# Performance work log

Hardware: AMD Instinct MI355X
Metric: run time of the kernel (lower is better)

The kernel has to match this reference:

```python
import jax, jax.numpy as jnp
import numpy as np

B, S, D, H = 4, 2048, 1024, 16
DK = D // H


def setup_inputs() -> dict:
    key = jax.random.key(0)
    ks = jax.random.split(key, 5)
    scale = 1.0 / np.sqrt(D)
    return {
        "x": jax.random.normal(ks[0], (B, S, D), dtype=jnp.float32),
        "W_Q": jax.random.normal(ks[1], (D, D), dtype=jnp.float32) * scale,
        "W_K": jax.random.normal(ks[2], (D, D), dtype=jnp.float32) * scale,
        "W_V": jax.random.normal(ks[3], (D, D), dtype=jnp.float32) * scale,
        "W_O": jax.random.normal(ks[4], (D, D), dtype=jnp.float32) * scale,
    }


def reference(x, W_Q, W_K, W_V, W_O):
    b, s, d = x.shape
    # torch Linear convention: y = x @ W.T  (no bias in this assignment's Linear)
    q = (x @ W_Q.T).reshape(b, s, H, DK).transpose(0, 2, 1, 3)  # [b,h,s,dk]
    k = (x @ W_K.T).reshape(b, s, H, DK).transpose(0, 2, 1, 3)
    v = (x @ W_V.T).reshape(b, s, H, DK).transpose(0, 2, 1, 3)
    scores = jnp.einsum("bhqd,bhkd->bhqk", q, k) / jnp.sqrt(jnp.float32(DK))
    causal = jnp.tril(jnp.ones((s, s), dtype=bool))  # True where attention allowed
    scores = jnp.where(causal, scores, jnp.finfo(scores.dtype).min)
    attn = jax.nn.softmax(scores, axis=-1)
    out = jnp.einsum("bhqk,bhkd->bhqd", attn, v)
    out = out.transpose(0, 2, 1, 3).reshape(b, s, d)
    return out @ W_O.T
```

## Files before the change

### kernel.cpp

```cpp
#include <hip/hip_runtime.h>
#include <hip/hip_bf16.h>

#define BB 4
#define SS 2048
#define DD 1024
#define HH 16
#define DKK 64

typedef __attribute__((ext_vector_type(8))) short short8;
typedef __attribute__((ext_vector_type(4))) float f32x4;

typedef const __attribute__((address_space(1))) void gvoid;
typedef __attribute__((address_space(3))) void lvoid;

__device__ __forceinline__ unsigned short f2bf(float f) {
  unsigned int u = __builtin_bit_cast(unsigned int, f);
  u = (u + 0x7FFFu + ((u >> 16) & 1u)) >> 16;
  return (unsigned short)u;
}

__global__ __launch_bounds__(256) void convert_f32_bf16(
    const float* __restrict__ in, unsigned short* __restrict__ out, int n4) {
  int i = blockIdx.x * blockDim.x + threadIdx.x;
  if (i >= n4) return;
  float4 v = reinterpret_cast<const float4*>(in)[i];
  ushort4 o;
  o.x = f2bf(v.x); o.y = f2bf(v.y); o.z = f2bf(v.z); o.w = f2bf(v.w);
  reinterpret_cast<ushort4*>(out)[i] = o;
}

template<int MODE>
__global__ __launch_bounds__(256) void gemm_bt(
    const unsigned short* __restrict__ A,
    const unsigned short* __restrict__ Bm,
    void* __restrict__ C,
    int M, int N, int K, float scale)
{
  __shared__ unsigned short As[128 * 32];
  __shared__ unsigned short Bs[128 * 32];
  int bid = blockIdx.x;
  int ntn = N >> 7;
  int m0 = (bid / ntn) << 7;
  int n0 = (bid % ntn) << 7;
  int t = threadIdx.x;
  int lane = t & 63, w = t >> 6;
  int l16 = lane & 15, lhi = lane >> 4;
  int wm = (w >> 1) * 64, wn = (w & 1) * 64;

  f32x4 acc[4][4];
#pragma unroll
  for (int i = 0; i < 4; ++i)
#pragma unroll
    for (int j = 0; j < 4; ++j) acc[i][j] = (f32x4){0.f, 0.f, 0.f, 0.f};

  for (int kt = 0; kt < K; kt += 32) {
    __syncthreads();
#pragma unroll
    for (int is = 0; is < 2; ++is) {
      int c = is * 256 + t;
      __builtin_amdgcn_global_load_lds(
          (gvoid*)(A + (size_t)(m0 + (c >> 2)) * K + kt + ((c & 3) << 3)),
          (lvoid*)(As + (size_t)(is * 256 + w * 64) * 8), 16, 0, 0);
      __builtin_amdgcn_global_load_lds(
          (gvoid*)(Bm + (size_t)(n0 + (c >> 2)) * K + kt + ((c & 3) << 3)),
          (lvoid*)(Bs + (size_t)(is * 256 + w * 64) * 8), 16, 0, 0);
    }
    __syncthreads();
    short8 af[4], bfr[4];
#pragma unroll
    for (int mf = 0; mf < 4; ++mf)
      af[mf] = *(const short8*)(As + (wm + mf * 16 + l16) * 32 + lhi * 8);
#pragma unroll
    for (int nf = 0; nf < 4; ++nf)
      bfr[nf] = *(const short8*)(Bs + (wn + nf * 16 + l16) * 32 + lhi * 8);
#pragma unroll
    for (int mf = 0; mf < 4; ++mf)
#pragma unroll
      for (int nf = 0; nf < 4; ++nf)
        acc[mf][nf] = __builtin_amdgcn_mfma_f32_16x16x32_bf16(
            af[mf], bfr[nf], acc[mf][nf], 0, 0, 0);
  }

  if (MODE == 0) {
    unsigned short* out = (unsigned short*)C;
#pragma unroll
    for (int mf = 0; mf < 4; ++mf)
#pragma unroll
      for (int nf = 0; nf < 4; ++nf)
#pragma unroll
        for (int i = 0; i < 4; ++i) {
          int r = m0 + wm + mf * 16 + lhi * 4 + i;
          int cc = n0 + wn + nf * 16 + l16;
          int b = r >> 11, s = r & 2047;
          int h = cc >> 6, dk = cc & 63;
          out[((size_t)((b * HH + h) * SS + s) << 6) + dk] =
              f2bf(acc[mf][nf][i] * scale);
        }
  } else if (MODE == 2) {
    unsigned short* out = (unsigned short*)C;
#pragma unroll
    for (int mf = 0; mf < 4; ++mf)
#pragma unroll
      for (int nf = 0; nf < 4; ++nf)
#pragma unroll
        for (int i = 0; i < 4; ++i) {
          int r = m0 + wm + mf * 16 + lhi * 4 + i;
          int cc = n0 + wn + nf * 16 + l16;
          int b = r >> 11, s = r & 2047;
          int h = cc >> 6, dk = cc & 63;
          out[(size_t)((b * HH + h) * DKK + dk) * SS + s] =
              f2bf(acc[mf][nf][i] * scale);
        }
  } else {
    float* out = (float*)C;
#pragma unroll
    for (int mf = 0; mf < 4; ++mf)
#pragma unroll
      for (int nf = 0; nf < 4; ++nf)
#pragma unroll
        for (int i = 0; i < 4; ++i) {
          int r = m0 + wm + mf * 16 + lhi * 4 + i;
          int cc = n0 + wn + nf * 16 + l16;
          out[(size_t)r * N + cc] = acc[mf][nf][i];
        }
  }
}

__global__ __launch_bounds__(256, 2) void attn_kernel(
    const unsigned short* __restrict__ Qh,
    const unsigned short* __restrict__ Kh,
    const unsigned short* __restrict__ Vt,
    unsigned short* __restrict__ O)
{
  __shared__ unsigned short Plds[4][32 * 72];

  int bid = blockIdx.x;
  int bh = bid & 63;
  int qb = 15 - (bid >> 6);
  int q0 = qb << 7;
  int t = threadIdx.x, lane = t & 63, w = t >> 6;
  int l16 = lane & 15, lhi = lane >> 4;
  int wq0 = q0 + w * 32;

  const unsigned short* Qb = Qh + (size_t)bh * SS * DKK;
  const unsigned short* Kb = Kh + (size_t)bh * SS * DKK;
  const unsigned short* Vb = Vt + (size_t)bh * SS * DKK;

  short8 aq[2][2];
#pragma unroll
  for (int qf = 0; qf < 2; ++qf)
#pragma unroll
    for (int kc = 0; kc < 2; ++kc)
      aq[qf][kc] = *(const short8*)(Qb + (size_t)(wq0 + qf * 16 + l16) * DKK +
                                    kc * 32 + lhi * 8);

  f32x4 oacc[2][4], acc1[2];
#pragma unroll
  for (int qf = 0; qf < 2; ++qf) {
    acc1[qf] = (f32x4){0.f, 0.f, 0.f, 0.f};
#pragma unroll
    for (int d = 0; d < 4; ++d) oacc[qf][d] = (f32x4){0.f, 0.f, 0.f, 0.f};
  }

  short8 ones;
  {
    short ov = (l16 == 0) ? (short)0x3F80 : (short)0;
#pragma unroll
    for (int j = 0; j < 8; ++j) ones[j] = ov;
  }

  int nt = (wq0 >> 6) + 1;

  short8 bk[4][2], bv[4][2];
#pragma unroll
  for (int sf = 0; sf < 4; ++sf)
#pragma unroll
    for (int kc = 0; kc < 2; ++kc)
      bk[sf][kc] = *(const short8*)(Kb + (size_t)(sf * 16 + l16) * DKK +
                                    kc * 32 + lhi * 8);
#pragma unroll
  for (int d = 0; d < 4; ++d)
#pragma unroll
    for (int kc = 0; kc < 2; ++kc)
      bv[d][kc] = *(const short8*)(Vb + (size_t)(d * 16 + l16) * SS +
                                   kc * 32 + lhi * 8);

  for (int tt = 0; tt < nt; ++tt) {
    int kv0 = tt << 6;
    f32x4 sacc[2][4];
#pragma unroll
    for (int qf = 0; qf < 2; ++qf)
#pragma unroll
      for (int sf = 0; sf < 4; ++sf) {
        sacc[qf][sf] = (f32x4){0.f, 0.f, 0.f, 0.f};
        sacc[qf][sf] = __builtin_amdgcn_mfma_f32_16x16x32_bf16(
            aq[qf][0], bk[sf][0], sacc[qf][sf], 0, 0, 0);
        sacc[qf][sf] = __builtin_amdgcn_mfma_f32_16x16x32_bf16(
            aq[qf][1], bk[sf][1], sacc[qf][sf], 0, 0, 0);
      }
    if (tt + 1 < nt) {
      int nk = kv0 + 64;
#pragma unroll
      for (int sf = 0; sf < 4; ++sf)
#pragma unroll
        for (int kc = 0; kc < 2; ++kc)
          bk[sf][kc] = *(const short8*)(Kb + (size_t)(nk + sf * 16 + l16) * DKK +
                                        kc * 32 + lhi * 8);
    }
    bool lastT = (tt == nt - 1);
#pragma unroll
    for (int qf = 0; qf < 2; ++qf)
#pragma unroll
      for (int sf = 0; sf < 4; ++sf)
#pragma unroll
        for (int i = 0; i < 4; ++i) {
          float p = exp2f(sacc[qf][sf][i] - 16.0f);
          if (lastT) {
            int key = kv0 + sf * 16 + l16;
            int qr = wq0 + qf * 16 + lhi * 4 + i;
            if (key > qr) p = 0.f;
          }
          Plds[w][(qf * 16 + lhi * 4 + i) * 72 + sf * 16 + l16] = f2bf(p);
        }
    short8 ap[2][2];
#pragma unroll
    for (int qf = 0; qf < 2; ++qf)
#pragma unroll
      for (int kc = 0; kc < 2; ++kc)
        ap[qf][kc] = *(const short8*)(&Plds[w][(qf * 16 + l16) * 72 + kc * 32 + lhi * 8]);
#pragma unroll
    for (int qf = 0; qf < 2; ++qf)
#pragma unroll
      for (int kc = 0; kc < 2; ++kc)
        acc1[qf] = __builtin_amdgcn_mfma_f32_16x16x32_bf16(
            ap[qf][kc], ones, acc1[qf], 0, 0, 0);
#pragma unroll
    for (int qf = 0; qf < 2; ++qf)
#pragma unroll
      for (int d = 0; d < 4; ++d)
#pragma unroll
        for (int kc = 0; kc < 2; ++kc)
          oacc[qf][d] = __builtin_amdgcn_mfma_f32_16x16x32_bf16(
              ap[qf][kc], bv[d][kc], oacc[qf][d], 0, 0, 0);
    if (tt + 1 < nt) {
      int nk = kv0 + 64;
#pragma unroll
      for (int d = 0; d < 4; ++d)
#pragma unroll
        for (int kc = 0; kc < 2; ++kc)
          bv[d][kc] = *(const short8*)(Vb + (size_t)(d * 16 + l16) * SS + nk +
                                       kc * 32 + lhi * 8);
    }
  }

  int b = bh >> 4, h = bh & 15;
#pragma unroll
  for (int qf = 0; qf < 2; ++qf)
#pragma unroll
    for (int i = 0; i < 4; ++i) {
      float l = __shfl(acc1[qf][i], lane & 48);
      float inv = 1.0f / l;
      int s = wq0 + qf * 16 + lhi * 4 + i;
#pragma unroll
      for (int d = 0; d < 4; ++d)
        O[(size_t)(b * SS + s) * DD + h * DKK + d * 16 + l16] =
            f2bf(oacc[qf][d][i] * inv);
    }
}

extern "C" void kernel_launch(void* const* d_in, const int* in_sizes, int n_in,
                              void* d_out, int out_size, void* d_ws, size_t ws_size,
                              hipStream_t stream) {
  const float* x  = (const float*)d_in[0];
  const float* WQ = (const float*)d_in[1];
  const float* WK = (const float*)d_in[2];
  const float* WV = (const float*)d_in[3];
  const float* WO = (const float*)d_in[4];
  float* out = (float*)d_out;

  const size_t NX = (size_t)BB * SS * DD;
  const size_t NW = (size_t)DD * DD;

  unsigned short* xb = (unsigned short*)d_ws;
  unsigned short* wq = xb + NX;
  unsigned short* wk = wq + NW;
  unsigned short* wv = wk + NW;
  unsigned short* wo = wv + NW;
  unsigned short* Qh = wo + NW;
  unsigned short* Kh = Qh + NX;
  unsigned short* Vt = Kh + NX;
  unsigned short* attn = Vt + NX;

  convert_f32_bf16<<<(int)(NX / 4 / 256), 256, 0, stream>>>(x, xb, (int)(NX / 4));
  convert_f32_bf16<<<(int)(NW / 4 / 256), 256, 0, stream>>>(WQ, wq, (int)(NW / 4));
  convert_f32_bf16<<<(int)(NW / 4 / 256), 256, 0, stream>>>(WK, wk, (int)(NW / 4));
  convert_f32_bf16<<<(int)(NW / 4 / 256), 256, 0, stream>>>(WV, wv, (int)(NW / 4));
  convert_f32_bf16<<<(int)(NW / 4 / 256), 256, 0, stream>>>(WO, wo, (int)(NW / 4));

  const int M = BB * SS;
  gemm_bt<0><<<(M / 128) * (DD / 128), 256, 0, stream>>>(xb, wq, Qh, M, DD, DD,
                                                         0.18033688011112042f);
  gemm_bt<0><<<(M / 128) * (DD / 128), 256, 0, stream>>>(xb, wk, Kh, M, DD, DD, 1.0f);
  gemm_bt<2><<<(M / 128) * (DD / 128), 256, 0, stream>>>(xb, wv, Vt, M, DD, DD, 1.0f);

  attn_kernel<<<BB * HH * (SS / 128), 256, 0, stream>>>(Qh, Kh, Vt, attn);

  gemm_bt<1><<<(M / 128) * (DD / 128), 256, 0, stream>>>(attn, wo, out, M, DD, DD, 1.0f);
}
```

Before: 358.7 us.

## Fuse QKV GEMMs and weight conversions; rebalance causal attention with 16-row paired strips

The four weight conversions become one launch, and the three Q/K/V projection GEMMs become one GEMM over concatenated weights (N=3072), which cuts launch overhead and gives the grid more blocks. The attention kernel now gives each wave 16-row query strips, pairing strip a with strip 127-a so every wave does the same amount of causal work. Each block holds fewer registers, so the launch bound rises to four blocks per SM. The smaller per-wave tile reuses each K/V register load across fewer query rows, so memory traffic per unit of compute goes up.

New measurement: 480.2 us. 33.9% more time.

```diff
diff --git a/kernel.cpp b/kernel.cpp
--- a/kernel.cpp
+++ b/kernel.cpp
@@ -29,12 +29,99 @@
   reinterpret_cast<ushort4*>(out)[i] = o;
 }
 
-template<int MODE>
-__global__ __launch_bounds__(256) void gemm_bt(
+__global__ __launch_bounds__(256) void convert_w4(
+    const float* __restrict__ a, const float* __restrict__ b,
+    const float* __restrict__ c, const float* __restrict__ d,
+    unsigned short* __restrict__ out, int n4) {
+  int m = blockIdx.y;
+  const float* src = (m == 0) ? a : (m == 1) ? b : (m == 2) ? c : d;
+  int i = blockIdx.x * blockDim.x + threadIdx.x;
+  if (i >= n4) return;
+  float4 v = reinterpret_cast<const float4*>(src)[i];
+  ushort4 o;
+  o.x = f2bf(v.x); o.y = f2bf(v.y); o.z = f2bf(v.z); o.w = f2bf(v.w);
+  reinterpret_cast<ushort4*>(out)[(size_t)m * n4 + i] = o;
+}
+
+__global__ __launch_bounds__(256) void gemm_qkv(
     const unsigned short* __restrict__ A,
     const unsigned short* __restrict__ Bm,
-    void* __restrict__ C,
-    int M, int N, int K, float scale)
+    unsigned short* __restrict__ Qo,
+    unsigned short* __restrict__ Ko,
+    unsigned short* __restrict__ Vo)
+{
+  __shared__ unsigned short As[128 * 32];
+  __shared__ unsigned short Bs[128 * 32];
+  const int K = DD;
+  int bid = blockIdx.x;
+  int m0 = (bid / 24) << 7;
+  int n0 = (bid % 24) << 7;
+  int t = threadIdx.x;
+  int lane = t & 63, w = t >> 6;
+  int l16 = lane & 15, lhi = lane >> 4;
+  int wm = (w >> 1) * 64, wn = (w & 1) * 64;
+
+  f32x4 acc[4][4];
+#pragma unroll
+  for (int i = 0; i < 4; ++i)
+#pragma unroll
+    for (int j = 0; j < 4; ++j) acc[i][j] = (f32x4){0.f, 0.f, 0.f, 0.f};
+
+  for (int kt = 0; kt < K; kt += 32) {
+    __syncthreads();
+#pragma unroll
+    for (int is = 0; is < 2; ++is) {
+      int c = is * 256 + t;
+      __builtin_amdgcn_global_load_lds(
+          (gvoid*)(A + (size_t)(m0 + (c >> 2)) * K + kt + ((c & 3) << 3)),
+          (lvoid*)(As + (size_t)(is * 256 + w * 64) * 8), 16, 0, 0);
+      __builtin_amdgcn_global_load_lds(
+          (gvoid*)(Bm + (size_t)(n0 + (c >> 2)) * K + kt + ((c & 3) << 3)),
+          (lvoid*)(Bs + (size_t)(is * 256 + w * 64) * 8), 16, 0, 0);
+    }
+    __syncthreads();
+    short8 af[4], bfr[4];
+#pragma unroll
+    for (int mf = 0; mf < 4; ++mf)
+      af[mf] = *(const short8*)(As + (wm + mf * 16 + l16) * 32 + lhi * 8);
+#pragma unroll
+    for (int nf = 0; nf < 4; ++nf)
+      bfr[nf] = *(const short8*)(Bs + (wn + nf * 16 + l16) * 32 + lhi * 8);
+#pragma unroll
+    for (int mf = 0; mf < 4; ++mf)
+#pragma unroll
+      for (int nf = 0; nf < 4; ++nf)
+        acc[mf][nf] = __builtin_amdgcn_mfma_f32_16x16x32_bf16(
+            af[mf], bfr[nf], acc[mf][nf], 0, 0, 0);
+  }
+
+  int mat = n0 >> 10;
+  int nb = n0 & 1023;
+  const float qscale = 0.18033688011112042f;
+#pragma unroll
+  for (int mf = 0; mf < 4; ++mf)
+#pragma unroll
+    for (int nf = 0; nf < 4; ++nf)
+#pragma unroll
+      for (int i = 0; i < 4; ++i) {
+        int r = m0 + wm + mf * 16 + lhi * 4 + i;
+        int c1 = nb + wn + nf * 16 + l16;
+        int b = r >> 11, s = r & 2047;
+        int h = c1 >> 6, dk = c1 & 63;
+        if (mat == 0)
+          Qo[((size_t)((b * HH + h) * SS + s) << 6) + dk] =
+              f2bf(acc[mf][nf][i] * qscale);
+        else if (mat == 1)
+          Ko[((size_t)((b * HH + h) * SS + s) << 6) + dk] = f2bf(acc[mf][nf][i]);
+        else
+          Vo[(size_t)((b * HH + h) * DKK + dk) * SS + s] = f2bf(acc[mf][nf][i]);
+      }
+}
+
+__global__ __launch_bounds__(256) void gemm_wo(
+    const unsigned short* __restrict__ A,
+    const unsigned short* __restrict__ Bm,
+    float* __restrict__ C, int N, int K)
 {
   __shared__ unsigned short As[128 * 32];
   __shared__ unsigned short Bs[128 * 32];
@@ -81,86 +168,37 @@
             af[mf], bfr[nf], acc[mf][nf], 0, 0, 0);
   }
 
-  if (MODE == 0) {
-    unsigned short* out = (unsigned short*)C;
-#pragma unroll
-    for (int mf = 0; mf < 4; ++mf)
-#pragma unroll
-      for (int nf = 0; nf < 4; ++nf)
-#pragma unroll
-        for (int i = 0; i < 4; ++i) {
-          int r = m0 + wm + mf * 16 + lhi * 4 + i;
-          int cc = n0 + wn + nf * 16 + l16;
-          int b = r >> 11, s = r & 2047;
-          int h = cc >> 6, dk = cc & 63;
-          out[((size_t)((b * HH + h) * SS + s) << 6) + dk] =
-              f2bf(acc[mf][nf][i] * scale);
-        }
-  } else if (MODE == 2) {
-    unsigned short* out = (unsigned short*)C;
-#pragma unroll
-    for (int mf = 0; mf < 4; ++mf)
-#pragma unroll
-      for (int nf = 0; nf < 4; ++nf)
-#pragma unroll
-        for (int i = 0; i < 4; ++i) {
-          int r = m0 + wm + mf * 16 + lhi * 4 + i;
-          int cc = n0 + wn + nf * 16 + l16;
-          int b = r >> 11, s = r & 2047;
-          int h = cc >> 6, dk = cc & 63;
-          out[(size_t)((b * HH + h) * DKK + dk) * SS + s] =
-              f2bf(acc[mf][nf][i] * scale);
-        }
-  } else {
-    float* out = (float*)C;
-#pragma unroll
-    for (int mf = 0; mf < 4; ++mf)
-#pragma unroll
-      for (int nf = 0; nf < 4; ++nf)
-#pragma unroll
-        for (int i = 0; i < 4; ++i) {
-          int r = m0 + wm + mf * 16 + lhi * 4 + i;
-          int cc = n0 + wn + nf * 16 + l16;
-          out[(size_t)r * N + cc] = acc[mf][nf][i];
-        }
-  }
-}
-
-__global__ __launch_bounds__(256, 2) void attn_kernel(
+#pragma unroll
+  for (int mf = 0; mf < 4; ++mf)
+#pragma unroll
+    for (int nf = 0; nf < 4; ++nf)
+#pragma unroll
+      for (int i = 0; i < 4; ++i) {
+        int r = m0 + wm + mf * 16 + lhi * 4 + i;
+        int cc = n0 + wn + nf * 16 + l16;
+        C[(size_t)r * N + cc] = acc[mf][nf][i];
+      }
+}
+
+__global__ __launch_bounds__(256, 4) void attn_kernel(
     const unsigned short* __restrict__ Qh,
     const unsigned short* __restrict__ Kh,
     const unsigned short* __restrict__ Vt,
     unsigned short* __restrict__ O)
 {
-  __shared__ unsigned short Plds[4][32 * 72];
+  __shared__ unsigned short Plds[4][16 * 72];
 
   int bid = blockIdx.x;
   int bh = bid & 63;
-  int qb = 15 - (bid >> 6);
-  int q0 = qb << 7;
+  int g = bid >> 6;
   int t = threadIdx.x, lane = t & 63, w = t >> 6;
   int l16 = lane & 15, lhi = lane >> 4;
-  int wq0 = q0 + w * 32;
+  int a = g * 4 + w;
 
   const unsigned short* Qb = Qh + (size_t)bh * SS * DKK;
   const unsigned short* Kb = Kh + (size_t)bh * SS * DKK;
   const unsigned short* Vb = Vt + (size_t)bh * SS * DKK;
-
-  short8 aq[2][2];
-#pragma unroll
-  for (int qf = 0; qf < 2; ++qf)
-#pragma unroll
-    for (int kc = 0; kc < 2; ++kc)
-      aq[qf][kc] = *(const short8*)(Qb + (size_t)(wq0 + qf * 16 + l16) * DKK +
-                                    kc * 32 + lhi * 8);
-
-  f32x4 oacc[2][4], acc1[2];
-#pragma unroll
-  for (int qf = 0; qf < 2; ++qf) {
-    acc1[qf] = (f32x4){0.f, 0.f, 0.f, 0.f};
-#pragma unroll
-    for (int d = 0; d < 4; ++d) oacc[qf][d] = (f32x4){0.f, 0.f, 0.f, 0.f};
-  }
+  int b = bh >> 4, h = bh & 15;
 
   short8 ones;
   {
@@ -169,103 +207,103 @@
     for (int j = 0; j < 8; ++j) ones[j] = ov;
   }
 
-  int nt = (wq0 >> 6) + 1;
-
-  short8 bk[4][2], bv[4][2];
-#pragma unroll
-  for (int sf = 0; sf < 4; ++sf)
+  for (int half = 0; half < 2; ++half) {
+    int strip = half ? (127 - a) : a;
+    int wq0 = strip << 4;
+    int nt = (wq0 >> 6) + 1;
+
+    short8 aq[2];
 #pragma unroll
     for (int kc = 0; kc < 2; ++kc)
-      bk[sf][kc] = *(const short8*)(Kb + (size_t)(sf * 16 + l16) * DKK +
-                                    kc * 32 + lhi * 8);
-#pragma unroll
-  for (int d = 0; d < 4; ++d)
-#pragma unroll
-    for (int kc = 0; kc < 2; ++kc)
-      bv[d][kc] = *(const short8*)(Vb + (size_t)(d * 16 + l16) * SS +
-                                   kc * 32 + lhi * 8);
-
-  for (int tt = 0; tt < nt; ++tt) {
-    int kv0 = tt << 6;
-    f32x4 sacc[2][4];
-#pragma unroll
-    for (int qf = 0; qf < 2; ++qf)
+      aq[kc] = *(const short8*)(Qb + (size_t)(wq0 + l16) * DKK + kc * 32 + lhi * 8);
+
+    f32x4 oacc[4], acc1;
+    acc1 = (f32x4){0.f, 0.f, 0.f, 0.f};
+#pragma unroll
+    for (int d = 0; d < 4; ++d) oacc[d] = (f32x4){0.f, 0.f, 0.f, 0.f};
+
+    short8 bk[4][2], bv[4][2];
+#pragma unroll
+    for (int sf = 0; sf < 4; ++sf)
+#pragma unroll
+      for (int kc = 0; kc < 2; ++kc)
+        bk[sf][kc] = *(const short8*)(Kb + (size_t)(sf * 16 + l16) * DKK +
+                                      kc * 32 + lhi * 8);
+#pragma unroll
+    for (int d = 0; d < 4; ++d)
+#pragma unroll
+      for (int kc = 0; kc < 2; ++kc)
+        bv[d][kc] = *(const short8*)(Vb + (size_t)(d * 16 + l16) * SS +
+                                     kc * 32 + lhi * 8);
+
+    for (int tt = 0; tt < nt; ++tt) {
+      int kv0 = tt << 6;
+      f32x4 sacc[4];
 #pragma unroll
       for (int sf = 0; sf < 4; ++sf) {
-        sacc[qf][sf] = (f32x4){0.f, 0.f, 0.f, 0.f};
-        sacc[qf][sf] = __builtin_amdgcn_mfma_f32_16x16x32_bf16(
-            aq[qf][0], bk[sf][0], sacc[qf][sf], 0, 0, 0);
-        sacc[qf][sf] = __builtin_amdgcn_mfma_f32_16x16x32_bf16(
-            aq[qf][1], bk[sf][1], sacc[qf][sf], 0, 0, 0);
-      }
-    if (tt + 1 < nt) {
-      int nk = kv0 + 64;
+        sacc[sf] = (f32x4){0.f, 0.f, 0.f, 0.f};
+        sacc[sf] = __builtin_amdgcn_mfma_f32_16x16x32_bf16(
+            aq[0], bk[sf][0], sacc[sf], 0, 0, 0);
+        sacc[sf] = __builtin_amdgcn_mfma_f32_16x16x32_bf16(
+            aq[1], bk[sf][1], sacc[sf], 0, 0, 0);
+      }
+      if (tt + 1 < nt) {
+        int nk = kv0 + 64;
+#pragma unroll
+        for (int sf = 0; sf < 4; ++sf)
+#pragma unroll
+          for (int kc = 0; kc < 2; ++kc)
+            bk[sf][kc] = *(const short8*)(Kb + (size_t)(nk + sf * 16 + l16) * DKK +
+                                          kc * 32 + lhi * 8);
+      }
+      bool lastT = (tt == nt - 1);
 #pragma unroll
       for (int sf = 0; sf < 4; ++sf)
 #pragma unroll
-        for (int kc = 0; kc < 2; ++kc)
-          bk[sf][kc] = *(const short8*)(Kb + (size_t)(nk + sf * 16 + l16) * DKK +
-                                        kc * 32 + lhi * 8);
-    }
-    bool lastT = (tt == nt - 1);
-#pragma unroll
-    for (int qf = 0; qf < 2; ++qf)
-#pragma unroll
-      for (int sf = 0; sf < 4; ++sf)
-#pragma unroll
         for (int i = 0; i < 4; ++i) {
-          float p = exp2f(sacc[qf][sf][i] - 16.0f);
+          float p = exp2f(sacc[sf][i] - 16.0f);
           if (lastT) {
             int key = kv0 + sf * 16 + l16;
-            int qr = wq0 + qf * 16 + lhi * 4 + i;
+            int qr = wq0 + lhi * 4 + i;
             if (key > qr) p = 0.f;
           }
-          Plds[w][(qf * 16 + lhi * 4 + i) * 72 + sf * 16 + l16] = f2bf(p);
+          Plds[w][(lhi * 4 + i) * 72 + sf * 16 + l16] = f2bf(p);
         }
-    short8 ap[2][2];
-#pragma unroll
-    for (int qf = 0; qf < 2; ++qf)
+      short8 ap[2];
 #pragma unroll
       for (int kc = 0; kc < 2; ++kc)
-        ap[qf][kc] = *(const short8*)(&Plds[w][(qf * 16 + l16) * 72 + kc * 32 + lhi * 8]);
-#pragma unroll
-    for (int qf = 0; qf < 2; ++qf)
+        ap[kc] = *(const short8*)(&Plds[w][l16 * 72 + kc * 32 + lhi * 8]);
 #pragma unroll
       for (int kc = 0; kc < 2; ++kc)
-        acc1[qf] = __builtin_amdgcn_mfma_f32_16x16x32_bf16(
-            ap[qf][kc], ones, acc1[qf], 0, 0, 0);
-#pragma unroll
-    for (int qf = 0; qf < 2; ++qf)
+        acc1 = __builtin_amdgcn_mfma_f32_16x16x32_bf16(ap[kc], ones, acc1, 0, 0, 0);
 #pragma unroll
       for (int d = 0; d < 4; ++d)
 #pragma unroll
         for (int kc = 0; kc < 2; ++kc)
-          oacc[qf][d] = __builtin_amdgcn_mfma_f32_16x16x32_bf16(
-              ap[qf][kc], bv[d][kc], oacc[qf][d], 0, 0, 0);
-    if (tt + 1 < nt) {
-      int nk = kv0 + 64;
+          oacc[d] = __builtin_amdgcn_mfma_f32_16x16x32_bf16(
+              ap[kc], bv[d][kc], oacc[d], 0, 0, 0);
+      if (tt + 1 < nt) {
+        int nk = kv0 + 64;
+#pragma unroll
+        for (int d = 0; d < 4; ++d)
+#pragma unroll
+          for (int kc = 0; kc < 2; ++kc)
+            bv[d][kc] = *(const short8*)(Vb + (size_t)(d * 16 + l16) * SS + nk +
+                                         kc * 32 + lhi * 8);
+      }
+    }
+
+#pragma unroll
+    for (int i = 0; i < 4; ++i) {
+      float l = __shfl(acc1[i], lane & 48);
+      float inv = 1.0f / l;
+      int s = wq0 + lhi * 4 + i;
 #pragma unroll
       for (int d = 0; d < 4; ++d)
-#pragma unroll
-        for (int kc = 0; kc < 2; ++kc)
-          bv[d][kc] = *(const short8*)(Vb + (size_t)(d * 16 + l16) * SS + nk +
-                                       kc * 32 + lhi * 8);
+        O[(size_t)(b * SS + s) * DD + h * DKK + d * 16 + l16] =
+            f2bf(oacc[d][i] * inv);
     }
   }
-
-  int b = bh >> 4, h = bh & 15;
-#pragma unroll
-  for (int qf = 0; qf < 2; ++qf)
-#pragma unroll
-    for (int i = 0; i < 4; ++i) {
-      float l = __shfl(acc1[qf][i], lane & 48);
-      float inv = 1.0f / l;
-      int s = wq0 + qf * 16 + lhi * 4 + i;
-#pragma unroll
-      for (int d = 0; d < 4; ++d)
-        O[(size_t)(b * SS + s) * DD + h * DKK + d * 16 + l16] =
-            f2bf(oacc[qf][d][i] * inv);
-    }
 }
 
 extern "C" void kernel_launch(void* const* d_in, const int* in_sizes, int n_in,
@@ -281,29 +319,21 @@
   const size_t NX = (size_t)BB * SS * DD;
   const size_t NW = (size_t)DD * DD;
 
-  unsigned short* xb = (unsigned short*)d_ws;
-  unsigned short* wq = xb + NX;
-  unsigned short* wk = wq + NW;
-  unsigned short* wv = wk + NW;
-  unsigned short* wo = wv + NW;
-  unsigned short* Qh = wo + NW;
-  unsigned short* Kh = Qh + NX;
-  unsigned short* Vt = Kh + NX;
+  unsigned short* xb   = (unsigned short*)d_ws;
+  unsigned short* wcat = xb + NX;
+  unsigned short* wo   = wcat + 3 * NW;
+  unsigned short* Qh   = wcat + 4 * NW;
+  unsigned short* Kh   = Qh + NX;
+  unsigned short* Vt   = Kh + NX;
   unsigned short* attn = Vt + NX;
 
   convert_f32_bf16<<<(int)(NX / 4 / 256), 256, 0, stream>>>(x, xb, (int)(NX / 4));
-  convert_f32_bf16<<<(int)(NW / 4 / 256), 256, 0, stream>>>(WQ, wq, (int)(NW / 4));
-  convert_f32_bf16<<<(int)(NW / 4 / 256), 256, 0, stream>>>(WK, wk, (int)(NW / 4));
-  convert_f32_bf16<<<(int)(NW / 4 / 256), 256, 0, stream>>>(WV, wv, (int)(NW / 4));
-  convert_f32_bf16<<<(int)(NW / 4 / 256), 256, 0, stream>>>(WO, wo, (int)(NW / 4));
-
-  const int M = BB * SS;
-  gemm_bt<0><<<(M / 128) * (DD / 128), 256, 0, stream>>>(xb, wq, Qh, M, DD, DD,
-                                                         0.18033688011112042f);
-  gemm_bt<0><<<(M / 128) * (DD / 128), 256, 0, stream>>>(xb, wk, Kh, M, DD, DD, 1.0f);
-  gemm_bt<2><<<(M / 128) * (DD / 128), 256, 0, stream>>>(xb, wv, Vt, M, DD, DD, 1.0f);
+  convert_w4<<<dim3((unsigned)(NW / 4 / 256), 4), 256, 0, stream>>>(
+      WQ, WK, WV, WO, wcat, (int)(NW / 4));
+
+  gemm_qkv<<<64 * 24, 256, 0, stream>>>(xb, wcat, Qh, Kh, Vt);
 
   attn_kernel<<<BB * HH * (SS / 128), 256, 0, stream>>>(Qh, Kh, Vt, attn);
 
-  gemm_bt<1><<<(M / 128) * (DD / 128), 256, 0, stream>>>(attn, wo, out, M, DD, DD, 1.0f);
-}
+  gemm_wo<<<64 * 8, 256, 0, stream>>>(attn, wo, out, DD, DD);
+}
```
